# Performance work log

Measured on AMD Instinct MI355X. Metric: run time of the kernel, lower is better.

## Reference

```python
import jax, jax.numpy as jnp
import numpy as np

NUM_USERS = 10000
NUM_POIS = 50000
SEQ_LEN = 100
EMB = 128
HEADS = 8
NUM_NODES = NUM_USERS + NUM_POIS + 1  # +1 padding node (last row)
N_LOCAL = 2
N_GLOBAL = 2
B = 1024
NNZ_G = 1920000
NNZ_H = 1600000


def spmm(rows, cols, vals, x, n):
    # torch.sparse.mm(COO, x): gather rows of x by cols, scale, scatter-add by rows
    return jax.ops.segment_sum(vals[:, None] * x[cols], rows, num_segments=n)


def mha(x, in_w, in_b, out_w, out_b):
    # torch.nn.MultiheadAttention (batch_first, eval mode, self-attention)
    b, l, d = x.shape
    hd = d // HEADS
    qkv = x @ in_w.T + in_b  # [b, l, 3d]
    q, k, v = jnp.split(qkv, 3, axis=-1)
    def split_heads(t):
        return t.reshape(b, l, HEADS, hd).transpose(0, 2, 1, 3)  # [b,h,l,hd]
    q, k, v = split_heads(q), split_heads(k), split_heads(v)
    scores = jnp.einsum('bhqd,bhkd->bhqk', q, k) / jnp.sqrt(jnp.asarray(hd, x.dtype))
    attn = jax.nn.softmax(scores, axis=-1)
    o = jnp.einsum('bhqk,bhkd->bhqd', attn, v)
    o = o.transpose(0, 2, 1, 3).reshape(b, l, d)
    return o @ out_w.T + out_b


def setup_inputs():
    key = jax.random.key(0)
    ks = jax.random.split(key, 32)
    stdv = 1.0 / np.sqrt(EMB)
    def u(k, shape):
        return jax.random.uniform(k, shape, jnp.float32, -stdv, stdv)
    inp = {}
    # --- learned parameters ---
    inp['nodes_emb'] = u(ks[0], (NUM_NODES, EMB)).at[NUM_NODES - 1].set(0.0)  # padding_idx
    inp['pos_emb_local'] = u(ks[1], (SEQ_LEN + 1, EMB)).at[0].set(0.0)
    inp['fc_geo_w'] = u(ks[2], (EMB, EMB))
    inp['fc_geo_b'] = u(ks[3], (EMB,))
    inp['in_proj_w'] = u(ks[4], (3 * EMB, EMB))
    inp['in_proj_b'] = u(ks[5], (3 * EMB,))
    inp['out_proj_w'] = u(ks[6], (EMB, EMB))
    inp['out_proj_b'] = u(ks[7], (EMB,))
    inp['pos_emb_glob'] = u(ks[8], (SEQ_LEN + 1, EMB)).at[0].set(0.0)
    inp['w1_w'] = u(ks[9], (EMB, 2 * EMB))
    inp['w1_b'] = u(ks[10], (EMB,))
    inp['w_2'] = u(ks[11], (EMB, 1))
    inp['glu1_w'] = u(ks[12], (EMB, EMB))
    inp['glu1_b'] = u(ks[13], (EMB,))
    inp['glu2_w'] = u(ks[14], (EMB, EMB))
    # --- sparse graphs (COO) ---
    inp['G_rows'] = jax.random.randint(ks[15], (NNZ_G,), 0, NUM_NODES - 1, jnp.int32)
    inp['G_cols'] = jax.random.randint(ks[16], (NNZ_G,), 0, NUM_NODES - 1, jnp.int32)
    inp['G_vals'] = jax.random.uniform(ks[17], (NNZ_G,), jnp.float32) * (1.0 / 32.0)
    inp['HG_rows'] = jax.random.randint(ks[18], (NNZ_H,), 0, NUM_POIS, jnp.int32)
    inp['HG_cols'] = jax.random.randint(ks[19], (NNZ_H,), 0, NUM_POIS, jnp.int32)
    inp['HG_vals'] = jax.random.uniform(ks[20], (NNZ_H,), jnp.float32) * (1.0 / 32.0)
    # --- batch tensors ---
    inp['batch_users_seqs'] = jax.random.randint(ks[21], (B, SEQ_LEN), 0, NUM_NODES - 1, jnp.int32)
    inp['batch_users_seqs_masks'] = jax.random.randint(ks[22], (B, SEQ_LEN), 0, 2, jnp.int32)
    inp['batch_users_geo_adjs'] = jax.random.uniform(ks[23], (B, SEQ_LEN, SEQ_LEN), jnp.float32) * (1.0 / SEQ_LEN)
    inp['batch_users_indices'] = jnp.arange(B, dtype=jnp.int32)
    inp['batch_seqs_lens'] = 1.0 + jax.random.uniform(ks[24], (B,), jnp.float32) * (SEQ_LEN - 1)
    inp['batch_users_rev_seqs'] = jax.random.randint(ks[25], (B, SEQ_LEN), 0, NUM_NODES - 1, jnp.int32)
    return inp


def reference(nodes_emb, pos_emb_local, fc_geo_w, fc_geo_b, in_proj_w, in_proj_b,
              out_proj_w, out_proj_b, pos_emb_glob, w1_w, w1_b, w_2, glu1_w, glu1_b,
              glu2_w, G_rows, G_cols, G_vals, HG_rows, HG_cols, HG_vals,
              batch_users_seqs, batch_users_seqs_masks, batch_users_geo_adjs,
              batch_users_indices, batch_seqs_lens, batch_users_rev_seqs):
    pos_local = pos_emb_local[jnp.arange(1, SEQ_LEN + 1)]  # [L, D], same for all batches

    def st_layer(nodes):
        seq_e = nodes[batch_users_seqs]  # [B, L, D] gather
        geo_e = jnp.einsum('bls,bsd->bld', batch_users_geo_adjs, seq_e)
        geo_e = jax.nn.relu(geo_e @ fc_geo_w.T + fc_geo_b)
        tot = seq_e + pos_local[None] + geo_e
        o = mha(tot, in_proj_w, in_proj_b, out_proj_w, out_proj_b)
        users = jnp.mean(o, axis=1)  # [B, D]
        nodes = nodes.at[batch_users_indices].set(users)  # scatter
        core = spmm(G_rows, G_cols, G_vals, nodes[:-1], NUM_NODES - 1)
        return nodes.at[:-1].set(core)

    # local spatial-temporal graph: shared layer applied N_LOCAL times, layer-mean
    nodes = nodes_emb
    acc = nodes
    for _ in range(N_LOCAL):
        nodes = st_layer(nodes)
        acc = acc + nodes
    local = acc / (N_LOCAL + 1)

    local_users = local[batch_users_indices]
    local_pois = local[NUM_USERS:-1]

    # global hypergraph convolution on POI embeddings, layer-mean
    x = nodes_emb[NUM_USERS:-1]
    acc_g = x
    for _ in range(N_GLOBAL):
        x = spmm(HG_rows, HG_cols, HG_vals, x, NUM_POIS)
        acc_g = acc_g + x
    global_pois = acc_g / (N_GLOBAL + 1)

    pois_embs = local_pois + global_pois
    fusion = jnp.concatenate([local[:NUM_USERS], pois_embs,
                              jnp.zeros((1, EMB), local.dtype)], axis=0)

    # user temporal preference augmentation
    seq_h = fusion[batch_users_rev_seqs]  # [B, L, D]
    hs = jnp.sum(seq_h, axis=1) / batch_seqs_lens[:, None]  # [B, D]
    pos_idx = jnp.arange(1, SEQ_LEN + 1, dtype=jnp.int32)[None] * batch_users_seqs_masks
    pos_e = pos_emb_glob[pos_idx]  # [B, L, D]; masked positions hit padding row 0
    nh = jnp.tanh(jnp.concatenate([pos_e, seq_h], axis=-1) @ w1_w.T + w1_b)
    nh = jax.nn.sigmoid(nh @ glu1_w.T + glu1_b + hs[:, None, :] @ glu2_w.T)
    beta = nh @ w_2  # [B, L, 1]
    select = jnp.sum(beta * seq_h, axis=1)  # [B, D]

    batch_users_embs = select + local_users
    return batch_users_embs, pois_embs
```

## Files before the change

kernel.cpp:

```cpp
#include <hip/hip_runtime.h>
#include <hip/hip_bf16.h>
#include <math.h>

typedef __hip_bfloat16 bf16;

__device__ __forceinline__ float b2f(bf16 x){ return __bfloat162float(x); }
__device__ __forceinline__ bf16  f2b(float x){ return __float2bfloat16(x); }

__device__ __forceinline__ short f2bs(float f){
    unsigned u = __float_as_uint(f);
    u += 0x7fffu + ((u >> 16) & 1u);
    return (short)(u >> 16);
}
__device__ __forceinline__ float bs2f(short s){
    return __uint_as_float(((unsigned)(unsigned short)s) << 16);
}

#define NUSERS   10000
#define NPOIS    50000
#define SEQL     100
#define NNODES   60001
#define BATCH    1024
#define NNZG     1920000
#define NNZH     1600000
#define BL       (BATCH*SEQL)
#define BLD      (BL*128)
#define NND      (NNODES*128)
#define CN       (60000*128)
#define PD       (NPOIS*128)

__device__ __forceinline__ void  stc(bf16* p,  float v){ *p = f2b(v); }
__device__ __forceinline__ void  stc(float* p, float v){ *p = v; }

typedef __attribute__((ext_vector_type(8))) short s16x8;
typedef __attribute__((ext_vector_type(4))) float f32x4;

__global__ __launch_bounds__(256) void k_zero(float* __restrict__ p, int n4){
    int i = blockIdx.x*256 + threadIdx.x;
    if (i < n4) ((float4*)p)[i] = make_float4(0.f,0.f,0.f,0.f);
}

__global__ __launch_bounds__(256) void k_copy16(ulong2* __restrict__ dst,
                                                const ulong2* __restrict__ src, int n16){
    int i = blockIdx.x*256 + threadIdx.x;
    if (i < n16) dst[i] = src[i];
}

__global__ __launch_bounds__(256) void k_init(bf16* __restrict__ nodes, float* __restrict__ acc,
                                              const float* __restrict__ src, int n){
    int i = blockIdx.x*256 + threadIdx.x;
    if (i >= n) return;
    float v = src[i];
    nodes[i] = f2b(v); acc[i] = v;
}

__global__ __launch_bounds__(256) void k_gather_f(float* __restrict__ dst,
                                                  const float* __restrict__ table,
                                                  const int* __restrict__ idx, int rows){
    int gid = blockIdx.x*256 + threadIdx.x;
    if (gid >= rows*128) return;
    int r = gid >> 7, c = gid & 127;
    dst[(size_t)r*128 + c] = table[(size_t)idx[r]*128 + c];
}

__global__ __launch_bounds__(256) void k_mgeo2(bf16* __restrict__ tot,
                                               const bf16* __restrict__ nodes,
                                               const int* __restrict__ seqs,
                                               const float* __restrict__ adj,
                                               const float* __restrict__ fcw,
                                               const float* __restrict__ fcb,
                                               const float* __restrict__ posl){
    __shared__ short st[128*104];
    __shared__ short gt[112*136];
    int b = blockIdx.x, tid = threadIdx.x;
    const int* sq = seqs + b*SEQL;
    for (int i = tid; i < SEQL*128; i += 256){
        int j = i >> 7, c = i & 127;
        st[c*104 + j] = ((const short*)nodes)[(size_t)sq[j]*128 + c];
    }
    for (int i = tid; i < 128*4; i += 256){ int c = i>>2, r = i&3; st[c*104 + 100 + r] = 0; }
    __syncthreads();
    int wv = tid>>6, lane = tid&63, lr = lane&15, lk = lane>>4;
    const s16x8 zf = {0,0,0,0,0,0,0,0};
    s16x8 bfr[2][4];
    #pragma unroll
    for (int t = 0; t < 2; t++){
        int nt = wv*2 + t;
        #pragma unroll
        for (int kc = 0; kc < 4; kc++)
            bfr[t][kc] = *(const s16x8*)&st[(nt*16+lr)*104 + kc*32 + lk*8];
    }
    const float* ab = adj + (size_t)b*SEQL*SEQL;
    for (int mt = 0; mt < 7; mt++){
        int ar = min(mt*16 + lr, SEQL-1);
        s16x8 ah[4], al[4];
        #pragma unroll
        for (int kc = 0; kc < 4; kc++){
            float av[8] = {0,0,0,0,0,0,0,0};
            if (kc < 3){
                const float* ap = ab + (size_t)ar*SEQL + kc*32 + lk*8;
                float4 a0 = *(const float4*)ap;
                float4 a1 = *(const float4*)(ap + 4);
                av[0]=a0.x; av[1]=a0.y; av[2]=a0.z; av[3]=a0.w;
                av[4]=a1.x; av[5]=a1.y; av[6]=a1.z; av[7]=a1.w;
            } else if (lk == 0){
                float4 a0 = *(const float4*)(ab + (size_t)ar*SEQL + 96);
                av[0]=a0.x; av[1]=a0.y; av[2]=a0.z; av[3]=a0.w;
            }
            s16x8 h = zf, l = zf;
            #pragma unroll
            for (int j = 0; j < 8; j++){
                short hb = f2bs(av[j]);
                h[j] = hb;
                l[j] = f2bs(av[j] - bs2f(hb));
            }
            ah[kc] = h; al[kc] = l;
        }
        f32x4 c0 = {0.f,0.f,0.f,0.f}, c1 = {0.f,0.f,0.f,0.f};
        #pragma unroll
        for (int kc = 0; kc < 4; kc++){
            c0 = __builtin_amdgcn_mfma_f32_16x16x32_bf16(ah[kc], bfr[0][kc], c0, 0,0,0);
            c0 = __builtin_amdgcn_mfma_f32_16x16x32_bf16(al[kc], bfr[0][kc], c0, 0,0,0);
            c1 = __builtin_amdgcn_mfma_f32_16x16x32_bf16(ah[kc], bfr[1][kc], c1, 0,0,0);
            c1 = __builtin_amdgcn_mfma_f32_16x16x32_bf16(al[kc], bfr[1][kc], c1, 0,0,0);
        }
        #pragma unroll
        for (int t = 0; t < 2; t++){
            f32x4 cc = t ? c1 : c0;
            int col = wv*32 + t*16 + lr;
            #pragma unroll
            for (int r = 0; r < 4; r++){
                int row = mt*16 + lk*4 + r;
                gt[row*136 + col] = f2bs(cc[r]);
            }
        }
    }
    s16x8 wh[2][4], wl[2][4];
    int n0 = wv*32;
    #pragma unroll
    for (int t = 0; t < 2; t++){
        #pragma unroll
        for (int ks = 0; ks < 4; ks++){
            const float* wp = fcw + (size_t)(n0 + t*16 + lr)*128 + ks*32 + lk*8;
            float4 w0 = *(const float4*)(wp);
            float4 w1 = *(const float4*)(wp + 4);
            float wf[8] = {w0.x,w0.y,w0.z,w0.w,w1.x,w1.y,w1.z,w1.w};
            s16x8 h, l;
            #pragma unroll
            for (int j = 0; j < 8; j++){
                short hb = f2bs(wf[j]);
                h[j] = hb;
                l[j] = f2bs(wf[j] - bs2f(hb));
            }
            wh[t][ks] = h; wl[t][ks] = l;
        }
    }
    __syncthreads();
    for (int mt = 0; mt < 7; mt++){
        s16x8 ah[4];
        #pragma unroll
        for (int ks = 0; ks < 4; ks++)
            ah[ks] = *(const s16x8*)&gt[(mt*16+lr)*136 + ks*32 + lk*8];
        f32x4 c0 = {0.f,0.f,0.f,0.f}, c1 = {0.f,0.f,0.f,0.f};
        #pragma unroll
        for (int ks = 0; ks < 4; ks++){
            c0 = __builtin_amdgcn_mfma_f32_16x16x32_bf16(ah[ks], wh[0][ks], c0, 0,0,0);
            c0 = __builtin_amdgcn_mfma_f32_16x16x32_bf16(ah[ks], wl[0][ks], c0, 0,0,0);
            c1 = __builtin_amdgcn_mfma_f32_16x16x32_bf16(ah[ks], wh[1][ks], c1, 0,0,0);
            c1 = __builtin_amdgcn_mfma_f32_16x16x32_bf16(ah[ks], wl[1][ks], c1, 0,0,0);
        }
        #pragma unroll
        for (int t = 0; t < 2; t++){
            f32x4 cc = t ? c1 : c0;
            int col = n0 + t*16 + lr;
            float bv = fcb[col];
            #pragma unroll
            for (int r = 0; r < 4; r++){
                int row = mt*16 + lk*4 + r;
                if (row < SEQL){
                    float v = fmaxf(cc[r] + bv, 0.f);
                    v += bs2f(st[col*104 + row]) + posl[(row+1)*128 + col];
                    tot[(size_t)b*SEQL*128 + (size_t)row*128 + col] = f2b(v);
                }
            }
        }
    }
}

template<typename TA, typename TC>
__global__ __launch_bounds__(256) void k_mgemm(const TA* __restrict__ A,
                                               const float* __restrict__ W, int wstride, int woff,
                                               const float* __restrict__ bias, int boff,
                                               TC* __restrict__ C, int act,
                                               const float* __restrict__ add1, int addmode,
                                               const int* __restrict__ masks,
                                               const int* __restrict__ outidx){
    constexpr bool A_BF = (sizeof(TA) == 2);
    int tid  = threadIdx.x;
    int wv   = tid >> 6;
    int lane = tid & 63;
    int lr   = lane & 15;
    int lk   = lane >> 4;
    int n0   = wv * 32;

    s16x8 wh[2][4], wl[2][4];
    #pragma unroll
    for (int t = 0; t < 2; t++){
        #pragma unroll
        for (int ks = 0; ks < 4; ks++){
            const float* wp = W + (size_t)(n0 + t*16 + lr)*wstride + woff + ks*32 + lk*8;
            float4 w0 = *(const float4*)(wp);
            float4 w1 = *(const float4*)(wp + 4);
            float wf[8] = {w0.x,w0.y,w0.z,w0.w,w1.x,w1.y,w1.z,w1.w};
            s16x8 h, l;
            #pragma unroll
            for (int j = 0; j < 8; j++){
                short hb = f2bs(wf[j]);
                h[j] = hb;
                l[j] = f2bs(wf[j] - bs2f(hb));
            }
            wh[t][ks] = h; wl[t][ks] = l;
        }
    }

    size_t mblk = (size_t)blockIdx.x * 128;
    for (int it = 0; it < 8; it++){
        size_t m0 = mblk + (size_t)it*16;
        s16x8 ah[4], al[4];
        #pragma unroll
        for (int ks = 0; ks < 4; ks++){
            if constexpr (A_BF){
                ah[ks] = *(const s16x8*)((const short*)A + (m0 + lr)*128 + ks*32 + lk*8);
            } else {
                const float* ap = (const float*)A + (m0 + lr)*128 + ks*32 + lk*8;
                float4 a0 = *(const float4*)(ap);
                float4 a1 = *(const float4*)(ap + 4);
                float av[8] = {a0.x,a0.y,a0.z,a0.w,a1.x,a1.y,a1.z,a1.w};
                s16x8 h, l;
                #pragma unroll
                for (int j = 0; j < 8; j++){
                    short hb = f2bs(av[j]);
                    h[j] = hb;
                    l[j] = f2bs(av[j] - bs2f(hb));
                }
                ah[ks] = h; al[ks] = l;
            }
        }
        __syncthreads();
        f32x4 c0 = {0.f,0.f,0.f,0.f}, c1 = {0.f,0.f,0.f,0.f};
        #pragma unroll
        for (int ks = 0; ks < 4; ks++){
            c0 = __builtin_amdgcn_mfma_f32_16x16x32_bf16(ah[ks], wh[0][ks], c0, 0, 0, 0);
            c0 = __builtin_amdgcn_mfma_f32_16x16x32_bf16(ah[ks], wl[0][ks], c0, 0, 0, 0);
            c1 = __builtin_amdgcn_mfma_f32_16x16x32_bf16(ah[ks], wh[1][ks], c1, 0, 0, 0);
            c1 = __builtin_amdgcn_mfma_f32_16x16x32_bf16(ah[ks], wl[1][ks], c1, 0, 0, 0);
            if constexpr (!A_BF){
                c0 = __builtin_amdgcn_mfma_f32_16x16x32_bf16(al[ks], wh[0][ks], c0, 0, 0, 0);
                c1 = __builtin_amdgcn_mfma_f32_16x16x32_bf16(al[ks], wh[1][ks], c1, 0, 0, 0);
            }
        }
        #pragma unroll
        for (int t = 0; t < 2; t++){
            f32x4 cc = t ? c1 : c0;
            int c = n0 + t*16 + lr;
            float bv = bias ? bias[boff + c] : 0.f;
            #pragma unroll
            for (int r4 = 0; r4 < 4; r4++){
                int m = (int)m0 + lk*4 + r4;
                float v = cc[r4] + bv;
                if (addmode == 1){
                    int l = m % SEQL;
                    int p = (l+1) * masks[m];
                    v += add1[p*128 + c];
                } else if (addmode == 2){
                    v += add1[(m/SEQL)*128 + c];
                }
                if (act == 1) v = fmaxf(v, 0.f);
                else if (act == 2) v = tanhf(v);
                else if (act == 3) v = 1.f/(1.f+__expf(-v));
                size_t orow = outidx ? (size_t)outidx[m] : (size_t)m;
                stc(&C[orow*128 + c], v);
            }
        }
    }
}

__global__ __launch_bounds__(256) void k_mattn(float* __restrict__ Omean,
                                               const bf16* __restrict__ Qq,
                                               const bf16* __restrict__ Qk,
                                               const bf16* __restrict__ Qv){
    __shared__ short Vt[128*104];
    __shared__ short Ph[4][16*136];
    __shared__ short Pl[4][16*136];
    int b = blockIdx.x, tid = threadIdx.x;
    const short* vsrc = (const short*)(Qv + (size_t)b*SEQL*128);
    for (int i = tid; i < SEQL*128; i += 256){ int j = i>>7, c = i&127; Vt[c*104 + j] = vsrc[i]; }
    for (int i = tid; i < 128*4; i += 256){ int c = i>>2, r = i&3; Vt[c*104 + 100 + r] = 0; }
    int wv = tid>>6, lane = tid&63, lr = lane&15, lk = lane>>4;
    short* phw = Ph[wv];
    short* plw = Pl[wv];
    for (int i = lane; i < 16*136; i += 64){ phw[i] = 0; plw[i] = 0; }
    __syncthreads();

    const s16x8 zf = {0,0,0,0,0,0,0,0};
    size_t rowbase = (size_t)b*SEQL*128;
    bool kreal = (lk < 2);
    for (int hh = 0; hh < 2; hh++){
        int h = wv*2 + hh;
        int hd = h*16 + lk*8;
        s16x8 kf[7];
        #pragma unroll
        for (int nt = 0; nt < 7; nt++){
            int kr = min(nt*16 + lr, SEQL-1);
            kf[nt] = kreal ? *(const s16x8*)((const short*)Qk + rowbase + (size_t)kr*128 + hd) : zf;
        }
        s16x8 vf[4];
        #pragma unroll
        for (int kc = 0; kc < 4; kc++)
            vf[kc] = *(const s16x8*)&Vt[(h*16+lr)*104 + kc*32 + lk*8];

        float msum = 0.f;
        for (int mt = 0; mt < 7; mt++){
            int qr = min(mt*16 + lr, SEQL-1);
            s16x8 qf = kreal ? *(const s16x8*)((const short*)Qq + rowbase + (size_t)qr*128 + hd) : zf;
            f32x4 sc[7];
            #pragma unroll
            for (int nt = 0; nt < 7; nt++){
                f32x4 z = {0.f,0.f,0.f,0.f};
                sc[nt] = __builtin_amdgcn_mfma_f32_16x16x32_bf16(qf, kf[nt], z, 0,0,0);
            }
            float mx[4] = {-1e30f,-1e30f,-1e30f,-1e30f};
            #pragma unroll
            for (int nt = 0; nt < 7; nt++){
                bool masked = (nt == 6) && (lr >= 4);
                #pragma unroll
                for (int r = 0; r < 4; r++){
                    float s = masked ? -1e30f : sc[nt][r]*0.25f;
                    sc[nt][r] = s;
                    mx[r] = fmaxf(mx[r], s);
                }
            }
            #pragma unroll
            for (int m = 1; m < 16; m <<= 1){
                #pragma unroll
                for (int r = 0; r < 4; r++) mx[r] = fmaxf(mx[r], __shfl_xor(mx[r], m));
            }
            float sm[4] = {0.f,0.f,0.f,0.f};
            #pragma unroll
            for (int nt = 0; nt < 7; nt++){
                #pragma unroll
                for (int r = 0; r < 4; r++){
                    float p = __expf(sc[nt][r] - mx[r]);
                    sc[nt][r] = p; sm[r] += p;
                }
            }
            #pragma unroll
            for (int m = 1; m < 16; m <<= 1){
                #pragma unroll
                for (int r = 0; r < 4; r++) sm[r] += __shfl_xor(sm[r], m);
            }
            float inv[4];
            #pragma unroll
            for (int r = 0; r < 4; r++) inv[r] = 1.f/sm[r];
            #pragma unroll
            for (int nt = 0; nt < 7; nt++){
                #pragma unroll
                for (int r = 0; r < 4; r++){
                    float p = sc[nt][r]*inv[r];
                    short hb = f2bs(p);
                    int pa = (lk*4+r)*136 + nt*16 + lr;
                    phw[pa] = hb;
                    plw[pa] = f2bs(p - bs2f(hb));
                }
            }
            f32x4 oa = {0.f,0.f,0.f,0.f};
            #pragma unroll
            for (int kc = 0; kc < 4; kc++){
                s16x8 pah = *(const s16x8*)&phw[lr*136 + kc*32 + lk*8];
                s16x8 pal = *(const s16x8*)&plw[lr*136 + kc*32 + lk*8];
                oa = __builtin_amdgcn_mfma_f32_16x16x32_bf16(pah, vf[kc], oa, 0,0,0);
                oa = __builtin_amdgcn_mfma_f32_16x16x32_bf16(pal, vf[kc], oa, 0,0,0);
            }
            #pragma unroll
            for (int r = 0; r < 4; r++){
                int row = mt*16 + lk*4 + r;
                if (row < SEQL) msum += oa[r];
            }
        }
        msum += __shfl_xor(msum, 16);
        msum += __shfl_xor(msum, 32);
        if (lk == 0) Omean[(size_t)b*128 + h*16 + lr] = msum * (1.f/(float)SEQL);
    }
}


__global__ __launch_bounds__(256) void k_hist(int* __restrict__ cnt,
                                              const int* __restrict__ rows, int nnz){
    int e = blockIdx.x*256 + threadIdx.x;
    if (e < nnz) atomicAdd(&cnt[rows[e]], 1);
}

__global__ __launch_bounds__(1024) void k_scan(int* __restrict__ cnt,
                                               int* __restrict__ rowptr, int nrows){
    __shared__ int part[1024];
    int tid = threadIdx.x;
    int chunk = (nrows + 1023) >> 10;
    int s = tid*chunk, e = min(s+chunk, nrows);
    int sum = 0;
    for (int i = s; i < e; i++) sum += cnt[i];
    part[tid] = sum;
    __syncthreads();
    for (int off = 1; off < 1024; off <<= 1){
        int add = (tid >= off) ? part[tid-off] : 0;
        __syncthreads();
        part[tid] += add;
        __syncthreads();
    }
    int run = part[tid] - sum;
    for (int i = s; i < e; i++){
        int c = cnt[i];
        rowptr[i] = run;
        cnt[i]    = run;
        run += c;
    }
    if (tid == 0) rowptr[nrows] = part[1023];
}

__global__ __launch_bounds__(256) void k_scatter(int2* __restrict__ cv,
                                                 int* __restrict__ cur,
                                                 const int* __restrict__ rows,
                                                 const int* __restrict__ cols,
                                                 const float* __restrict__ vals, int nnz){
    int e = blockIdx.x*256 + threadIdx.x;
    if (e >= nnz) return;
    int p = atomicAdd(&cur[rows[e]], 1);
    cv[p] = make_int2(cols[e], __float_as_int(vals[e]));
}

__global__ __launch_bounds__(256) void k_spmm_csr(bf16* __restrict__ yb,
                                                  float* __restrict__ acc,
                                                  const int* __restrict__ rowptr,
                                                  const int2* __restrict__ cv,
                                                  const bf16* __restrict__ x, int nrows){
    int row = blockIdx.x*4 + (threadIdx.x >> 6);
    if (row >= nrows) return;
    int lane = threadIdx.x & 63;
    int g = lane >> 3;
    int t = lane & 7;
    int s = rowptr[row], e = rowptr[row+1];
    float a[16];
    #pragma unroll
    for (int j = 0; j < 16; j++) a[j] = 0.f;
    for (int i = s + g; i < e; i += 8){
        int2 p = cv[i];
        float v = __int_as_float(p.y);
        const unsigned* xp = (const unsigned*)(x + (size_t)p.x*128 + t*16);
        uint4 u0 = *(const uint4*)xp;
        uint4 u1 = *(const uint4*)(xp + 4);
        unsigned w[8] = {u0.x,u0.y,u0.z,u0.w,u1.x,u1.y,u1.z,u1.w};
        #pragma unroll
        for (int j = 0; j < 8; j++){
            a[2*j]   += v * __uint_as_float((w[j] & 0xffffu) << 16);
            a[2*j+1] += v * __uint_as_float(w[j] & 0xffff0000u);
        }
    }
    #pragma unroll
    for (int j = 0; j < 16; j++){
        a[j] += __shfl_xor(a[j], 8);
        a[j] += __shfl_xor(a[j], 16);
        a[j] += __shfl_xor(a[j], 32);
    }
    if (g == 0){
        s16x8 o0, o1;
        #pragma unroll
        for (int j = 0; j < 8; j++){ o0[j] = f2bs(a[j]); o1[j] = f2bs(a[8+j]); }
        short* yp = (short*)yb + (size_t)row*128 + t*16;
        *(s16x8*)yp = o0;
        *(s16x8*)(yp + 8) = o1;
        float* ap = acc + (size_t)row*128 + t*16;
        #pragma unroll
        for (int q = 0; q < 4; q++){
            float4 c = ((float4*)ap)[q];
            c.x += a[q*4+0]; c.y += a[q*4+1]; c.z += a[q*4+2]; c.w += a[q*4+3];
            ((float4*)ap)[q] = c;
        }
    }
}

__global__ __launch_bounds__(256) void k_scale(float* __restrict__ a, int n){
    int i = blockIdx.x*256 + threadIdx.x;
    if (i < n) a[i] *= (1.f/3.f);
}

__global__ __launch_bounds__(256) void k_initg(bf16* __restrict__ xg, float* __restrict__ accg,
                                               const float* __restrict__ ne, int n){
    int i = blockIdx.x*256 + threadIdx.x;
    if (i >= n) return;
    float v = ne[(size_t)NUSERS*128 + i];
    xg[i] = f2b(v); accg[i] = v;
}

__global__ __launch_bounds__(256) void k_fusion(float* __restrict__ accP,
                                                const float* __restrict__ accg,
                                                float* __restrict__ outp, int n){
    int i = blockIdx.x*256 + threadIdx.x;
    if (i >= n) return;
    float v = accP[i] + accg[i]*(1.f/3.f);
    accP[i] = v;
    outp[i] = v;
}


__global__ __launch_bounds__(128) void k_hs(float* __restrict__ hs, const float* __restrict__ sh,
                                            const float* __restrict__ lens){
    int b = blockIdx.x, c = threadIdx.x;
    const float* p = sh + (size_t)b*SEQL*128 + c;
    float sum = 0.f;
    for (int l = 0; l < SEQL; l++) sum += p[l*128];
    hs[b*128 + c] = sum / lens[b];
}

__global__ __launch_bounds__(128) void k_posw(float* __restrict__ posW,
                                              const float* __restrict__ pg,
                                              const float* __restrict__ w1w){
    __shared__ float sm[128];
    int p = blockIdx.x, n = threadIdx.x;
    sm[n] = pg[p*128 + n];
    __syncthreads();
    const float* wr = w1w + (size_t)n*256;
    float s = 0.f;
    for (int k = 0; k < 128; k++) s += sm[k]*wr[k];
    posW[p*128 + n] = s;
}

__global__ __launch_bounds__(256) void k_beta(float* __restrict__ beta,
                                              const bf16* __restrict__ nh,
                                              const float* __restrict__ w2){
    int m = blockIdx.x*4 + (threadIdx.x >> 6);
    int lane = threadIdx.x & 63;
    float v = b2f(nh[(size_t)m*128 + lane]) * w2[lane]
            + b2f(nh[(size_t)m*128 + 64 + lane]) * w2[64 + lane];
    #pragma unroll
    for (int s = 1; s < 64; s <<= 1) v += __shfl_xor(v, s);
    if (lane == 0) beta[m] = v;
}

__global__ __launch_bounds__(128) void k_final(float* __restrict__ out,
                                               const float* __restrict__ beta,
                                               const float* __restrict__ seqh,
                                               const float* __restrict__ acc,
                                               const int* __restrict__ uidx){
    int b = blockIdx.x, c = threadIdx.x;
    const float* sh = seqh + (size_t)b*SEQL*128 + c;
    const float* bp = beta + b*SEQL;
    float sel = 0.f;
    for (int l = 0; l < SEQL; l++) sel += bp[l]*sh[l*128];
    out[b*128 + c] = sel + acc[(size_t)uidx[b]*128 + c];
}

extern "C" void kernel_launch(void* const* d_in, const int* in_sizes, int n_in,
                              void* d_out, int out_size, void* d_ws, size_t ws_size,
                              hipStream_t stream){
    const float* nodes_emb     = (const float*)d_in[0];
    const float* pos_emb_local = (const float*)d_in[1];
    const float* fc_geo_w      = (const float*)d_in[2];
    const float* fc_geo_b      = (const float*)d_in[3];
    const float* in_proj_w     = (const float*)d_in[4];
    const float* in_proj_b     = (const float*)d_in[5];
    const float* out_proj_w    = (const float*)d_in[6];
    const float* out_proj_b    = (const float*)d_in[7];
    const float* pos_emb_glob  = (const float*)d_in[8];
    const float* w1_w          = (const float*)d_in[9];
    const float* w1_b          = (const float*)d_in[10];
    const float* w_2           = (const float*)d_in[11];
    const float* glu1_w        = (const float*)d_in[12];
    const float* glu1_b        = (const float*)d_in[13];
    const float* glu2_w        = (const float*)d_in[14];
    const int*   G_rows        = (const int*)d_in[15];
    const int*   G_cols        = (const int*)d_in[16];
    const float* G_vals        = (const float*)d_in[17];
    const int*   HG_rows       = (const int*)d_in[18];
    const int*   HG_cols       = (const int*)d_in[19];
    const float* HG_vals       = (const float*)d_in[20];
    const int*   seqs          = (const int*)d_in[21];
    const int*   masks         = (const int*)d_in[22];
    const float* adjs          = (const float*)d_in[23];
    const int*   uidx          = (const int*)d_in[24];
    const float* lens          = (const float*)d_in[25];
    const int*   rev_seqs      = (const int*)d_in[26];
    float* out = (float*)d_out;

    char* base = (char*)d_ws;
    bf16*  nodes = (bf16*)base;
    float* acc   = (float*)(base + 15360256);
    char*  R     = base + 15360256 + 30720512;
    bf16* P1 = (bf16*)R;
    bf16* P2 = P1 + BLD;
    bf16* P3 = P2 + BLD;
    bf16*  xsnap = (bf16*)R;
    bf16*  xg     = (bf16*)R;
    bf16*  xsnapg = (bf16*)(R + 12800000);
    float* accg = (float*)(R + 12800000 + 25600000);
    int2*  Hcv  = (int2*)(R + 64000000);
    int*   Hptr = (int*)(R + 76800000);
    int*   Hcur = (int*)(R + 77000016);
    float* H1f  = (float*)R;
    bf16*  nh   = (bf16*)(R + 52428800);
    float* hs    = (float*)base;
    float* hproj = (float*)(base + 524288);
    float* posW  = (float*)(base + 1048576);
    float* betaB = (float*)(base + 1100288);
    char*  ob    = (char*)out;
    int2*  Gcv   = (int2*)ob;
    int*   Gptr  = (int*)(ob + 15360000);
    int*   Gcur  = (int*)(ob + 15600016);
    float* Omean = (float*)(ob + 15840016);

    auto gemm = [&](const bf16* A, const float* W, int wstride, int woff,
                    const float* bias, int boff, bf16* Cp, int act){
        k_mgemm<bf16,bf16><<<dim3(BL/128), dim3(256), 0, stream>>>(
            A, W, wstride, woff, bias, boff, Cp, act, nullptr, 0, nullptr, nullptr);
    };

    k_init<<<dim3((NND+255)/256), dim3(256), 0, stream>>>(nodes, acc, nodes_emb, NND);

    k_zero<<<dim3((15000+255)/256), dim3(256), 0, stream>>>((float*)Gcur, 15000);
    k_hist<<<dim3(NNZG/256), dim3(256), 0, stream>>>(Gcur, G_rows, NNZG);
    k_scan<<<dim3(1), dim3(1024), 0, stream>>>(Gcur, Gptr, 60000);
    k_scatter<<<dim3(NNZG/256), dim3(256), 0, stream>>>(Gcv, Gcur, G_rows, G_cols, G_vals, NNZG);

    for (int layer = 0; layer < 2; layer++){
        k_mgeo2<<<dim3(BATCH), dim3(256), 0, stream>>>(P3, nodes, seqs, adjs,
                                                       fc_geo_w, fc_geo_b, pos_emb_local);
        gemm(P3, in_proj_w, 128, 0,       in_proj_b, 0,   P1, 0);
        gemm(P3, in_proj_w, 128, 128*128, in_proj_b, 128, P2, 0);
        gemm(P3, in_proj_w, 128, 256*128, in_proj_b, 256, P3, 0);
        k_mattn<<<dim3(BATCH), dim3(256), 0, stream>>>(Omean, P1, P2, P3);
        k_mgemm<float,bf16><<<dim3(BATCH/128), dim3(256), 0, stream>>>(
            Omean, out_proj_w, 128, 0, out_proj_b, 0, nodes, 0, nullptr, 0, nullptr, uidx);
        k_copy16<<<dim3((960000+255)/256), dim3(256), 0, stream>>>(
            (ulong2*)xsnap, (const ulong2*)nodes, 960000);
        k_spmm_csr<<<dim3(60000/4), dim3(256), 0, stream>>>(nodes, acc, Gptr, Gcv, xsnap, 60000);
    }
    k_scale<<<dim3((NND+255)/256), dim3(256), 0, stream>>>(acc, NND);

    k_initg<<<dim3((PD+255)/256), dim3(256), 0, stream>>>(xg, accg, nodes_emb, PD);
    k_zero<<<dim3((12500+255)/256), dim3(256), 0, stream>>>((float*)Hcur, 12500);
    k_hist<<<dim3(NNZH/256), dim3(256), 0, stream>>>(Hcur, HG_rows, NNZH);
    k_scan<<<dim3(1), dim3(1024), 0, stream>>>(Hcur, Hptr, 50000);
    k_scatter<<<dim3(NNZH/256), dim3(256), 0, stream>>>(Hcv, Hcur, HG_rows, HG_cols, HG_vals, NNZH);
    for (int it = 0; it < 2; it++){
        k_copy16<<<dim3((800000+255)/256), dim3(256), 0, stream>>>(
            (ulong2*)xsnapg, (const ulong2*)xg, 800000);
        k_spmm_csr<<<dim3(50000/4), dim3(256), 0, stream>>>(xg, accg, Hptr, Hcv, xsnapg, 50000);
    }
    k_fusion<<<dim3((PD+255)/256), dim3(256), 0, stream>>>(acc + (size_t)NUSERS*128, accg, out + BATCH*128, PD);

    k_gather_f<<<dim3((BL*128+255)/256), dim3(256), 0, stream>>>(H1f, acc, rev_seqs, BL);
    k_hs<<<dim3(BATCH), dim3(128), 0, stream>>>(hs, H1f, lens);
    k_mgemm<float,float><<<dim3(BATCH/128), dim3(256), 0, stream>>>(
        hs, glu2_w, 128, 0, nullptr, 0, hproj, 0, nullptr, 0, nullptr, nullptr);
    k_posw<<<dim3(SEQL+1), dim3(128), 0, stream>>>(posW, pos_emb_glob, w1_w);
    k_mgemm<float,bf16><<<dim3(BL/128), dim3(256), 0, stream>>>(
        H1f, w1_w, 256, 128, w1_b, 0, nh, 2, posW, 1, masks, nullptr);
    k_mgemm<bf16,bf16><<<dim3(BL/128), dim3(256), 0, stream>>>(
        nh, glu1_w, 128, 0, glu1_b, 0, nh, 3, hproj, 2, nullptr, nullptr);
    k_beta<<<dim3(BL/4), dim3(256), 0, stream>>>(betaB, nh, w_2);
    k_final<<<dim3(BATCH), dim3(128), 0, stream>>>(out, betaB, H1f, acc, uidx);
}
```

Measured before the change: 1.968 ms.

## Two-pass bucketed COO-to-CSR scatter and fuse GLU sigmoid GEMM with beta reduction

COO-to-CSR conversion now runs in two passes. Entries are first appended into 16-row buckets via global atomics, then each bucket is placed into final CSR order with shared-memory atomics. This aims to cut global atomic contention and scattered writes. Separately, the second GLU GEMM (sigmoid) and the beta dot-product are fused into one MFMA kernel that never writes the nh intermediate and reduces straight to beta, at the cost of per-block shared atomics and syncs.

```diff
diff --git a/kernel.cpp b/kernel.cpp
--- a/kernel.cpp
+++ b/kernel.cpp
@@ -285,6 +285,86 @@
     }
 }
 
+__global__ __launch_bounds__(256) void k_nh2beta(const bf16* __restrict__ A,
+                                                 const float* __restrict__ W,
+                                                 const float* __restrict__ bias,
+                                                 const float* __restrict__ hproj,
+                                                 const float* __restrict__ w2,
+                                                 float* __restrict__ beta){
+    __shared__ float red[16];
+    int tid  = threadIdx.x;
+    int wv   = tid >> 6;
+    int lane = tid & 63;
+    int lr   = lane & 15;
+    int lk   = lane >> 4;
+    int n0   = wv * 32;
+
+    s16x8 wh[2][4], wl[2][4];
+    #pragma unroll
+    for (int t = 0; t < 2; t++){
+        #pragma unroll
+        for (int ks = 0; ks < 4; ks++){
+            const float* wp = W + (size_t)(n0 + t*16 + lr)*128 + ks*32 + lk*8;
+            float4 w0 = *(const float4*)(wp);
+            float4 w1 = *(const float4*)(wp + 4);
+            float wf[8] = {w0.x,w0.y,w0.z,w0.w,w1.x,w1.y,w1.z,w1.w};
+            s16x8 h, l;
+            #pragma unroll
+            for (int j = 0; j < 8; j++){
+                short hb = f2bs(wf[j]);
+                h[j] = hb;
+                l[j] = f2bs(wf[j] - bs2f(hb));
+            }
+            wh[t][ks] = h; wl[t][ks] = l;
+        }
+    }
+
+    size_t mblk = (size_t)blockIdx.x * 128;
+    for (int it = 0; it < 8; it++){
+        size_t m0 = mblk + (size_t)it*16;
+        s16x8 ah[4];
+        #pragma unroll
+        for (int ks = 0; ks < 4; ks++)
+            ah[ks] = *(const s16x8*)((const short*)A + (m0 + lr)*128 + ks*32 + lk*8);
+        if (tid < 16) red[tid] = 0.f;
+        __syncthreads();
+        f32x4 c0 = {0.f,0.f,0.f,0.f}, c1 = {0.f,0.f,0.f,0.f};
+        #pragma unroll
+        for (int ks = 0; ks < 4; ks++){
+            c0 = __builtin_amdgcn_mfma_f32_16x16x32_bf16(ah[ks], wh[0][ks], c0, 0, 0, 0);
+            c0 = __builtin_amdgcn_mfma_f32_16x16x32_bf16(ah[ks], wl[0][ks], c0, 0, 0, 0);
+            c1 = __builtin_amdgcn_mfma_f32_16x16x32_bf16(ah[ks], wh[1][ks], c1, 0, 0, 0);
+            c1 = __builtin_amdgcn_mfma_f32_16x16x32_bf16(ah[ks], wl[1][ks], c1, 0, 0, 0);
+        }
+        float pr[4] = {0.f,0.f,0.f,0.f};
+        #pragma unroll
+        for (int t = 0; t < 2; t++){
+            f32x4 cc = t ? c1 : c0;
+            int c = n0 + t*16 + lr;
+            float bv = bias[c];
+            float wc = w2[c];
+            #pragma unroll
+            for (int r4 = 0; r4 < 4; r4++){
+                int m = (int)m0 + lk*4 + r4;
+                float v = cc[r4] + bv + hproj[(m/SEQL)*128 + c];
+                v = 1.f/(1.f+__expf(-v));
+                pr[r4] += v * wc;
+            }
+        }
+        #pragma unroll
+        for (int s = 1; s < 16; s <<= 1){
+            #pragma unroll
+            for (int r4 = 0; r4 < 4; r4++) pr[r4] += __shfl_xor(pr[r4], s);
+        }
+        if (lr == 0){
+            #pragma unroll
+            for (int r4 = 0; r4 < 4; r4++) atomicAdd(&red[lk*4 + r4], pr[r4]);
+        }
+        __syncthreads();
+        if (tid < 16) beta[m0 + tid] = red[tid];
+    }
+}
+
 __global__ __launch_bounds__(256) void k_mattn(float* __restrict__ Omean,
                                                const bf16* __restrict__ Qq,
                                                const bf16* __restrict__ Qk,
@@ -426,15 +506,38 @@
     if (tid == 0) rowptr[nrows] = part[1023];
 }
 
-__global__ __launch_bounds__(256) void k_scatter(int2* __restrict__ cv,
-                                                 int* __restrict__ cur,
-                                                 const int* __restrict__ rows,
-                                                 const int* __restrict__ cols,
-                                                 const float* __restrict__ vals, int nnz){
+__global__ __launch_bounds__(256) void k_initcurB(int* __restrict__ curB,
+                                                  const int* __restrict__ rowptr, int nb){
+    int b = blockIdx.x*256 + threadIdx.x;
+    if (b < nb) curB[b] = rowptr[b << 4];
+}
+
+__global__ __launch_bounds__(256) void k_append(int2* __restrict__ stage,
+                                                int* __restrict__ curB,
+                                                const int* __restrict__ rows,
+                                                const int* __restrict__ cols,
+                                                const float* __restrict__ vals, int nnz){
     int e = blockIdx.x*256 + threadIdx.x;
     if (e >= nnz) return;
-    int p = atomicAdd(&cur[rows[e]], 1);
-    cv[p] = make_int2(cols[e], __float_as_int(vals[e]));
+    int r = rows[e];
+    int p = atomicAdd(&curB[r >> 4], 1);
+    stage[p] = make_int2(cols[e] | ((r & 15) << 17), __float_as_int(vals[e]));
+}
+
+__global__ __launch_bounds__(256) void k_place(int2* __restrict__ cv,
+                                               const int* __restrict__ rowptr,
+                                               const int2* __restrict__ stage, int nrows){
+    __shared__ int cur[16];
+    int b = blockIdx.x, tid = threadIdx.x;
+    int r0 = b << 4;
+    if (tid < 16) cur[tid] = rowptr[r0 + tid];
+    __syncthreads();
+    int s = rowptr[r0], e = rowptr[min(r0 + 16, nrows)];
+    for (int i = s + tid; i < e; i += 256){
+        int2 w = stage[i];
+        int p = atomicAdd(&cur[(w.x >> 17) & 15], 1);
+        cv[p] = make_int2(w.x & 0x1FFFF, w.y);
+    }
 }
 
 __global__ __launch_bounds__(256) void k_spmm_csr(bf16* __restrict__ yb,
@@ -531,18 +634,6 @@
     float s = 0.f;
     for (int k = 0; k < 128; k++) s += sm[k]*wr[k];
     posW[p*128 + n] = s;
-}
-
-__global__ __launch_bounds__(256) void k_beta(float* __restrict__ beta,
-                                              const bf16* __restrict__ nh,
-                                              const float* __restrict__ w2){
-    int m = blockIdx.x*4 + (threadIdx.x >> 6);
-    int lane = threadIdx.x & 63;
-    float v = b2f(nh[(size_t)m*128 + lane]) * w2[lane]
-            + b2f(nh[(size_t)m*128 + 64 + lane]) * w2[64 + lane];
-    #pragma unroll
-    for (int s = 1; s < 64; s <<= 1) v += __shfl_xor(v, s);
-    if (lane == 0) beta[m] = v;
 }
 
 __global__ __launch_bounds__(128) void k_final(float* __restrict__ out,
@@ -597,13 +688,16 @@
     bf16* P1 = (bf16*)R;
     bf16* P2 = P1 + BLD;
     bf16* P3 = P2 + BLD;
+    int2*  stageG = (int2*)R;
     bf16*  xsnap = (bf16*)R;
     bf16*  xg     = (bf16*)R;
     bf16*  xsnapg = (bf16*)(R + 12800000);
     float* accg = (float*)(R + 12800000 + 25600000);
-    int2*  Hcv  = (int2*)(R + 64000000);
-    int*   Hptr = (int*)(R + 76800000);
-    int*   Hcur = (int*)(R + 77000016);
+    int2*  Hcv   = (int2*)(R + 64000000);
+    int*   Hptr  = (int*)(R + 76800000);
+    int*   cntH  = (int*)(R + 77000016);
+    int*   curBH = (int*)(R + 77200016);
+    int2*  stageH = (int2*)out;
     float* H1f  = (float*)R;
     bf16*  nh   = (bf16*)(R + 52428800);
     float* hs    = (float*)base;
@@ -613,8 +707,9 @@
     char*  ob    = (char*)out;
     int2*  Gcv   = (int2*)ob;
     int*   Gptr  = (int*)(ob + 15360000);
-    int*   Gcur  = (int*)(ob + 15600016);
-    float* Omean = (float*)(ob + 15840016);
+    int*   cntG  = (int*)(ob + 15600016);
+    int*   curBG = (int*)(ob + 15840016);
+    float* Omean = (float*)(ob + 15856000);
 
     auto gemm = [&](const bf16* A, const float* W, int wstride, int woff,
                     const float* bias, int boff, bf16* Cp, int act){
@@ -624,10 +719,12 @@
 
     k_init<<<dim3((NND+255)/256), dim3(256), 0, stream>>>(nodes, acc, nodes_emb, NND);
 
-    k_zero<<<dim3((15000+255)/256), dim3(256), 0, stream>>>((float*)Gcur, 15000);
-    k_hist<<<dim3(NNZG/256), dim3(256), 0, stream>>>(Gcur, G_rows, NNZG);
-    k_scan<<<dim3(1), dim3(1024), 0, stream>>>(Gcur, Gptr, 60000);
-    k_scatter<<<dim3(NNZG/256), dim3(256), 0, stream>>>(Gcv, Gcur, G_rows, G_cols, G_vals, NNZG);
+    k_zero<<<dim3((15000+255)/256), dim3(256), 0, stream>>>((float*)cntG, 15000);
+    k_hist<<<dim3(NNZG/256), dim3(256), 0, stream>>>(cntG, G_rows, NNZG);
+    k_scan<<<dim3(1), dim3(1024), 0, stream>>>(cntG, Gptr, 60000);
+    k_initcurB<<<dim3(15), dim3(256), 0, stream>>>(curBG, Gptr, 3750);
+    k_append<<<dim3(NNZG/256), dim3(256), 0, stream>>>(stageG, curBG, G_rows, G_cols, G_vals, NNZG);
+    k_place<<<dim3(3750), dim3(256), 0, stream>>>(Gcv, Gptr, stageG, 60000);
 
     for (int layer = 0; layer < 2; layer++){
         k_mgeo2<<<dim3(BATCH), dim3(256), 0, stream>>>(P3, nodes, seqs, adjs,
@@ -645,10 +742,12 @@
     k_scale<<<dim3((NND+255)/256), dim3(256), 0, stream>>>(acc, NND);
 
     k_initg<<<dim3((PD+255)/256), dim3(256), 0, stream>>>(xg, accg, nodes_emb, PD);
-    k_zero<<<dim3((12500+255)/256), dim3(256), 0, stream>>>((float*)Hcur, 12500);
-    k_hist<<<dim3(NNZH/256), dim3(256), 0, stream>>>(Hcur, HG_rows, NNZH);
-    k_scan<<<dim3(1), dim3(1024), 0, stream>>>(Hcur, Hptr, 50000);
-    k_scatter<<<dim3(NNZH/256), dim3(256), 0, stream>>>(Hcv, Hcur, HG_rows, HG_cols, HG_vals, NNZH);
+    k_zero<<<dim3((12500+255)/256), dim3(256), 0, stream>>>((float*)cntH, 12500);
+    k_hist<<<dim3(NNZH/256), dim3(256), 0, stream>>>(cntH, HG_rows, NNZH);
+    k_scan<<<dim3(1), dim3(1024), 0, stream>>>(cntH, Hptr, 50000);
+    k_initcurB<<<dim3(13), dim3(256), 0, stream>>>(curBH, Hptr, 3125);
+    k_append<<<dim3(NNZH/256), dim3(256), 0, stream>>>(stageH, curBH, HG_rows, HG_cols, HG_vals, NNZH);
+    k_place<<<dim3(3125), dim3(256), 0, stream>>>(Hcv, Hptr, stageH, 50000);
     for (int it = 0; it < 2; it++){
         k_copy16<<<dim3((800000+255)/256), dim3(256), 0, stream>>>(
             (ulong2*)xsnapg, (const ulong2*)xg, 800000);
@@ -663,8 +762,6 @@
     k_posw<<<dim3(SEQL+1), dim3(128), 0, stream>>>(posW, pos_emb_glob, w1_w);
     k_mgemm<float,bf16><<<dim3(BL/128), dim3(256), 0, stream>>>(
         H1f, w1_w, 256, 128, w1_b, 0, nh, 2, posW, 1, masks, nullptr);
-    k_mgemm<bf16,bf16><<<dim3(BL/128), dim3(256), 0, stream>>>(
-        nh, glu1_w, 128, 0, glu1_b, 0, nh, 3, hproj, 2, nullptr, nullptr);
-    k_beta<<<dim3(BL/4), dim3(256), 0, stream>>>(betaB, nh, w_2);
+    k_nh2beta<<<dim3(BL/128), dim3(256), 0, stream>>>(nh, glu1_w, glu1_b, hproj, w_2, betaB);
     k_final<<<dim3(BATCH), dim3(128), 0, stream>>>(out, betaB, H1f, acc, uidx);
 }
```

New measurement: 1.990 ms. No clear change (+1.1%).
